# Performance work log

Measured on AMD Instinct MI355X. Metric: run time of the kernel, lower is better.

Reference implementation:

```python
import jax, jax.numpy as jnp
import numpy as np
import math

D_MODEL, N_HEADS, D_FF = 64, 8, 256
EPS = 1e-5


def _layernorm(x, w, b):
    mu = jnp.mean(x, axis=-1, keepdims=True)
    var = jnp.mean(jnp.square(x - mu), axis=-1, keepdims=True)
    return (x - mu) * jax.lax.rsqrt(var + EPS) * w + b


def setup_inputs() -> dict:
    key = jax.random.key(0)
    ks = jax.random.split(key, 16)
    B, S, D, F = 4, 2048, D_MODEL, D_FF
    s = 1.0 / math.sqrt(D)
    inp = {
        "x": jax.random.normal(ks[0], (B, S, D), jnp.float32),
        "mask": jax.random.randint(ks[1], (B, 1, S, S), 0, 2, jnp.int32),
        "Wq": jax.random.normal(ks[2], (D, D), jnp.float32) * s,
        "bq": jax.random.normal(ks[3], (D,), jnp.float32) * 0.02,
        "Wk": jax.random.normal(ks[4], (D, D), jnp.float32) * s,
        "bk": jax.random.normal(ks[5], (D,), jnp.float32) * 0.02,
        "Wv": jax.random.normal(ks[6], (D, D), jnp.float32) * s,
        "bv": jax.random.normal(ks[7], (D,), jnp.float32) * 0.02,
        "Wo": jax.random.normal(ks[8], (D, D), jnp.float32) * s,
        "bo": jax.random.normal(ks[9], (D,), jnp.float32) * 0.02,
        "W1": jax.random.normal(ks[10], (D, F), jnp.float32) * s,
        "b1": jax.random.normal(ks[11], (F,), jnp.float32) * 0.02,
        "W2": jax.random.normal(ks[12], (F, D), jnp.float32) * (1.0 / math.sqrt(F)),
        "b2": jax.random.normal(ks[13], (D,), jnp.float32) * 0.02,
        "ln1_w": jnp.ones((D,), jnp.float32),
        "ln1_b": jnp.zeros((D,), jnp.float32),
        "ln2_w": jnp.ones((D,), jnp.float32),
        "ln2_b": jnp.zeros((D,), jnp.float32),
    }
    return inp


def reference(x, mask, Wq, bq, Wk, bk, Wv, bv, Wo, bo, W1, b1, W2, b2,
              ln1_w, ln1_b, ln2_w, ln2_b):
    B, S, D = x.shape
    H = N_HEADS
    dk = D // H

    x1 = _layernorm(x, ln1_w, ln1_b)

    # [B,S,D] -> [B,H,S,dk]
    def heads(t):
        return t.reshape(B, S, H, dk).transpose(0, 2, 1, 3)

    Q = heads(x1 @ Wq + bq)
    K = heads(x1 @ Wk + bk)
    V = heads(x1 @ Wv + bv)

    scores = jnp.einsum("bhqd,bhkd->bhqk", Q, K) / math.sqrt(dk)
    scores = jnp.where(mask == 1, jnp.float32(-1e9), scores)
    attn = jax.nn.softmax(scores, axis=-1)
    ctx = jnp.einsum("bhqk,bhkd->bhqd", attn, V)
    # Faithful to source: view [B,H,S,dk] -> [B,S,D] WITHOUT transposing heads back.
    ctx = ctx.reshape(B, S, D)
    attn_out = ctx @ Wo + bo + x1  # residual added inside attention

    x2 = x1 + attn_out  # residual added again in the block (faithful double-add)
    x3 = _layernorm(x2, ln2_w, ln2_b)
    ff = jax.nn.gelu(x3 @ W1 + b1, approximate=False) @ W2 + b2
    return x2 + ff
```

## Files before the change

kernel.cpp:

```cpp
#include <hip/hip_runtime.h>
#include <hip/hip_bf16.h>

#define SEQ 2048

typedef short s4v __attribute__((ext_vector_type(4)));
typedef float f32x4 __attribute__((ext_vector_type(4)));

using bf16 = __hip_bfloat16;
using ull = unsigned long long;

#if __has_builtin(__builtin_amdgcn_exp2f)
#define EXP2(x) __builtin_amdgcn_exp2f(x)
#else
#define EXP2(x) exp2f(x)
#endif

__device__ __forceinline__ float wred_sum(float v){
#pragma unroll
  for (int i = 1; i < 64; i <<= 1) v += __shfl_xor(v, i, 64);
  return v;
}

__device__ __forceinline__ float wred_max(float v){
#pragma unroll
  for (int i = 1; i < 64; i <<= 1) v = fmaxf(v, __shfl_xor(v, i, 64));
  return v;
}

__device__ __forceinline__ short bfs(float f){
  bf16 h = __float2bfloat16(f);
  short s;
  __builtin_memcpy(&s, &h, 2);
  return s;
}

__device__ __forceinline__ unsigned bfs2(float a, float b){
  float2 t; t.x = a; t.y = b;
  __hip_bfloat162 h = __float22bfloat162_rn(t);
  unsigned u;
  __builtin_memcpy(&u, &h, 4);
  return u;
}

__device__ __forceinline__ int detect_f32(const void* xraw){
  const unsigned short* p = (const unsigned short*)xraw;
  const int lane = threadIdx.x & 63;
  float mx = 0.f;
#pragma unroll
  for (int i = 0; i < 2; ++i){
    unsigned u = ((unsigned)p[lane * 2 + i]) << 16;
    float f = fabsf(__uint_as_float(u));
    if (!(f < 1e30f)) f = 1e30f;
    mx = fmaxf(mx, f);
  }
  mx = wred_max(mx);
  return mx > 1e3f ? 1 : 0;
}

template<int F32>
__device__ __forceinline__ float ldf(const void* p, int i){
  if constexpr (F32) return ((const float*)p)[i];
  else return __bfloat162float(((const bf16*)p)[i]);
}

#define QSCALE 0.5101129340352065f

template<int F32>
__device__ __forceinline__ void ln_qkv_body(
    const void* x,
    const void* Wq, const void* bq,
    const void* Wk, const void* bk,
    const void* Wv, const void* bv,
    const void* ln1w, const void* ln1b,
    float* x1f, bf16* Qp, bf16* Kp, bf16* Vti, float (*xs)[64])
{
  const int w = threadIdx.x >> 6, lane = threadIdx.x & 63;
  const int row = (blockIdx.x - 2048) * 4 + w;
  float xv = ldf<F32>(x, row * 64 + lane);
  float mu = wred_sum(xv) * 0.015625f;
  float dv = xv - mu;
  float var = wred_sum(dv * dv) * 0.015625f;
  float x1 = dv * rsqrtf(var + 1e-5f) * ldf<F32>(ln1w, lane) + ldf<F32>(ln1b, lane);
  x1f[(size_t)row * 64 + lane] = x1;
  xs[w][lane] = x1;
  __syncthreads();
  float q = ldf<F32>(bq, lane);
  float k = ldf<F32>(bk, lane);
  float v = ldf<F32>(bv, lane);
#pragma unroll 16
  for (int d = 0; d < 64; ++d){
    float xd = xs[w][d];
    q += xd * ldf<F32>(Wq, d * 64 + lane);
    k += xd * ldf<F32>(Wk, d * 64 + lane);
    v += xd * ldf<F32>(Wv, d * 64 + lane);
  }
  const int bq_ = row >> 11, sq = row & 2047;
  const int hh = lane >> 3, dd = lane & 7;
  const int bh = bq_ * 8 + hh;
  const size_t pidx = ((size_t)bh * SEQ + sq) * 8 + dd;
  Qp[pidx] = __float2bfloat16(q * QSCALE);
  Kp[pidx] = __float2bfloat16(k);
  const int tt = sq >> 4, j = sq & 15;
  Vti[(((size_t)(bh * 128 + tt)) * 9 + dd) * 16 + j] = __float2bfloat16(v);
}

template<int F32>
__device__ __forceinline__ void wt_body(
    const void* Wo, const void* W1, const void* W2,
    bf16* WoT, bf16* W1T, bf16* W2T)
{
  const int idx = (blockIdx.x - 4096) * 256 + threadIdx.x;
  if (idx < 4096){
    const int c = idx >> 6, d = idx & 63;
    WoT[idx] = __float2bfloat16(ldf<F32>(Wo, d * 64 + c));
  } else if (idx < 20480){
    const int e = idx - 4096;
    const int f = e >> 6, d = e & 63;
    W1T[e] = __float2bfloat16(ldf<F32>(W1, d * 256 + f));
  } else {
    const int e = idx - 20480;
    const int c = e >> 8, f = e & 255;
    W2T[e] = __float2bfloat16(ldf<F32>(W2, f * 64 + c));
  }
}

__global__ __launch_bounds__(256) void k_prep(
    const int* __restrict__ mask, ull* __restrict__ pm,
    const void* x, const void* Wq, const void* bq, const void* Wk, const void* bk,
    const void* Wv, const void* bv, const void* ln1w, const void* ln1b,
    float* x1f, bf16* Qp, bf16* Kp, bf16* Vti,
    const void* Wo, const void* W1, const void* W2,
    bf16* WoT, bf16* W1T, bf16* W2T)
{
  __shared__ float xs[4][64];
  const int w = threadIdx.x >> 6, lane = threadIdx.x & 63;
  if (blockIdx.x < 2048){
    const int row = blockIdx.x * 4 + w;
    const int b = row >> 11, q = row & 2047;
    const int* rp = mask + (size_t)row * SEQ;
    ull* op = pm + ((size_t)(b * 128 + (q >> 4))) * 512 + (q & 15) * 2;
#pragma unroll
    for (int it = 0; it < 8; ++it){
      const int c0 = it * 256 + lane;
      ull m0 = __ballot(rp[c0] == 1);
      ull m1 = __ballot(rp[c0 + 64] == 1);
      ull m2 = __ballot(rp[c0 + 128] == 1);
      ull m3 = __ballot(rp[c0 + 192] == 1);
      if (lane == 0){
#pragma unroll
        for (int j = 0; j < 4; ++j){
          const int wi = it * 4 + j;
          const ull mv = (j == 0) ? m0 : (j == 1) ? m1 : (j == 2) ? m2 : m3;
          op[(wi >> 1) * 32 + (wi & 1)] = mv;
        }
      }
    }
    return;
  }
  if (blockIdx.x >= 4240){
    const int idx = (blockIdx.x - 4240) * 256 + threadIdx.x;
    const int bh = idx >> 11;
    const int rem = idx & 2047;
    const int tt = rem >> 4, j = rem & 15;
    Vti[(((size_t)(bh * 128 + tt)) * 9 + 8) * 16 + j] = __float2bfloat16(1.0f);
    return;
  }
  if (blockIdx.x >= 4096){
    if (detect_f32(x)) wt_body<1>(Wo, W1, W2, WoT, W1T, W2T);
    else               wt_body<0>(Wo, W1, W2, WoT, W1T, W2T);
    return;
  }
  if (detect_f32(x))
    ln_qkv_body<1>(x, Wq, bq, Wk, bk, Wv, bv, ln1w, ln1b, x1f, Qp, Kp, Vti, xs);
  else
    ln_qkv_body<0>(x, Wq, bq, Wk, bk, Wv, bv, ln1w, ln1b, x1f, Qp, Kp, Vti, xs);
}

#define LOADT(PB, T) do {                                                          \
    const int tt_ = (T);                                                           \
    _Pragma("unroll")                                                              \
    for (int i_ = 0; i_ < 8; ++i_){                                                \
      kf[PB][i_] = *reinterpret_cast<const s4v*>(kb8 + (size_t)(tt_ * 128 + i_ * 16) * 8); \
      vf[PB][i_] = *reinterpret_cast<const s4v*>(vb8 + (size_t)(tt_ * 8 + i_) * 144);      \
    }                                                                              \
    mwvA[PB] = pbA[tt_ * 16];                                                      \
    mwvB[PB] = pbB[tt_ * 16];                                                      \
  } while (0)

#define QTILE(PB, C, MM, QF, ACCA, ACCB) do {                                      \
    f32x4 st_[4];                                                                  \
    _Pragma("unroll")                                                              \
    for (int i_ = 0; i_ < 4; ++i_)                                                 \
      st_[i_] = __builtin_amdgcn_mfma_f32_16x16x16bf16_1k(kf[PB][(C) * 4 + i_], QF, zf, 0, 0, 0); \
    _Pragma("unroll")                                                              \
    for (int i_ = 0; i_ < 4; ++i_){                                                \
      const unsigned b4_ = (unsigned)((MM) >> (16 * i_ + sh4)) & 0xFu;             \
      float p0_ = (b4_ & 1u) ? 0.f : EXP2(st_[i_][0]);                             \
      float p1_ = (b4_ & 2u) ? 0.f : EXP2(st_[i_][1]);                             \
      float p2_ = (b4_ & 4u) ? 0.f : EXP2(st_[i_][2]);                             \
      float p3_ = (b4_ & 8u) ? 0.f : EXP2(st_[i_][3]);                             \
      union { unsigned u[2]; s4v s; } pu_;                                         \
      pu_.u[0] = bfs2(p0_, p1_);                                                   \
      pu_.u[1] = bfs2(p2_, p3_);                                                   \
      if (i_ & 1) ACCB = __builtin_amdgcn_mfma_f32_16x16x16bf16_1k(vf[PB][(C) * 4 + i_], pu_.s, ACCB, 0, 0, 0); \
      else        ACCA = __builtin_amdgcn_mfma_f32_16x16x16bf16_1k(vf[PB][(C) * 4 + i_], pu_.s, ACCA, 0, 0, 0); \
    }                                                                              \
  } while (0)

#define COMPT(PB) do {                                                             \
    const ull mxA_ = (((ull)mwvA[PB].y) << 32) | mwvA[PB].x;                       \
    const ull myA_ = (((ull)mwvA[PB].w) << 32) | mwvA[PB].z;                       \
    const ull mxB_ = (((ull)mwvB[PB].y) << 32) | mwvB[PB].x;                       \
    const ull myB_ = (((ull)mwvB[PB].w) << 32) | mwvB[PB].z;                       \
    QTILE(PB, 0, mxA_, qfA, accA0, accB0);                                         \
    QTILE(PB, 0, mxB_, qfB, accA1, accB1);                                         \
    QTILE(PB, 1, myA_, qfA, accA0, accB0);                                         \
    QTILE(PB, 1, myB_, qfB, accA1, accB1);                                         \
  } while (0)

__global__ __launch_bounds__(256, 4) void k_attn(
    const bf16* __restrict__ Qp, const bf16* __restrict__ Kp,
    const bf16* __restrict__ Vti, const uint4* __restrict__ pmi,
    bf16* __restrict__ ctxb)
{
  const int blk = blockIdx.x;
  const int h  = blk & 7;
  const int qt = (blk >> 3) & 63;
  const int b  = blk >> 9;
  const int kq = threadIdx.x >> 6;
  const int bh = b * 8 + h;
  const int q0 = qt * 32;
  const int lane = threadIdx.x & 63;
  const int g = lane >> 4, qi = lane & 15;
  const int sh4 = 4 * g;
  const int tbase = kq * 4;

  __shared__ float mlds[3][2][16][17];

  s4v qfA = {0, 0, 0, 0}, qfB = {0, 0, 0, 0};
  if (g < 2){
    qfA = *reinterpret_cast<const s4v*>(Qp + ((size_t)(bh * SEQ + q0 + qi)) * 8 + sh4);
    qfB = *reinterpret_cast<const s4v*>(Qp + ((size_t)(bh * SEQ + q0 + 16 + qi)) * 8 + sh4);
  }

  const bf16*  kb8 = Kp + ((size_t)bh * SEQ + qi) * 8 + sh4;
  const bf16*  vb8 = Vti + (size_t)bh * 128 * 144 + qi * 16 + sh4;
  const uint4* pbA = pmi + (size_t)(b * 128 + 2 * qt) * 256 + qi;
  const uint4* pbB = pbA + 256;

  f32x4 accA0 = {0.f, 0.f, 0.f, 0.f}, accB0 = {0.f, 0.f, 0.f, 0.f};
  f32x4 accA1 = {0.f, 0.f, 0.f, 0.f}, accB1 = {0.f, 0.f, 0.f, 0.f};
  const f32x4 zf = {0.f, 0.f, 0.f, 0.f};

  s4v kf[2][8], vf[2][8];
  uint4 mwvA[2], mwvB[2];

  LOADT(0, tbase);
  for (int it2 = 0; it2 < 2; ++it2){
    LOADT(1, tbase + ((2 * it2 + 1) & 3));
    COMPT(0);
    LOADT(0, tbase + ((2 * it2 + 2) & 3));
    COMPT(1);
  }

  f32x4 acc0, acc1;
#pragma unroll
  for (int r = 0; r < 4; ++r){
    acc0[r] = accA0[r] + accB0[r];
    acc1[r] = accA1[r] + accB1[r];
  }

  if (kq > 0){
#pragma unroll
    for (int r = 0; r < 4; ++r){
      mlds[kq - 1][0][4 * g + r][qi] = acc0[r];
      mlds[kq - 1][1][4 * g + r][qi] = acc1[r];
    }
  }
  __syncthreads();
  if (kq == 0){
#pragma unroll
    for (int j = 0; j < 3; ++j)
#pragma unroll
      for (int r = 0; r < 4; ++r){
        acc0[r] += mlds[j][0][4 * g + r][qi];
        acc1[r] += mlds[j][1][4 * g + r][qi];
      }
    const float s0 = __shfl(acc0[0], 32 + qi, 64);
    const float s1 = __shfl(acc1[0], 32 + qi, 64);
    if (g < 2){
      const float i0 = 1.f / s0, i1 = 1.f / s1;
      s4v oA, oB;
#pragma unroll
      for (int r = 0; r < 4; ++r){ oA[r] = bfs(acc0[r] * i0); oB[r] = bfs(acc1[r] * i1); }
      *reinterpret_cast<s4v*>(ctxb + ((size_t)(bh * SEQ + q0 + qi)) * 8 + sh4) = oA;
      *reinterpret_cast<s4v*>(ctxb + ((size_t)(bh * SEQ + q0 + 16 + qi)) * 8 + sh4) = oB;
    }
  }
}

template<int F32>
__device__ __forceinline__ void ffn_mfma_body(
    const bf16* __restrict__ ctxb, const float* __restrict__ x1f,
    const bf16* __restrict__ WoT, const bf16* __restrict__ W1T, const bf16* __restrict__ W2T,
    const void* bo, const void* b1, const void* b2,
    const void* ln2w, const void* ln2b, void* out)
{
  const int lane = threadIdx.x & 63;
  const int row0 = blockIdx.x * 16;
  const int xr = lane & 15;
  const int ko = (lane >> 4) * 4;
  const f32x4 zf = {0.f, 0.f, 0.f, 0.f};

  s4v cb[4];
#pragma unroll
  for (int kk = 0; kk < 4; ++kk)
    cb[kk] = *reinterpret_cast<const s4v*>(ctxb + (size_t)(row0 + xr) * 64 + kk * 16 + ko);

  float x2v[4][4];
#pragma unroll
  for (int t = 0; t < 4; ++t){
    f32x4 acc = zf;
#pragma unroll
    for (int kk = 0; kk < 4; ++kk){
      s4v a = *reinterpret_cast<const s4v*>(WoT + (size_t)(t * 16 + xr) * 64 + kk * 16 + ko);
      acc = __builtin_amdgcn_mfma_f32_16x16x16bf16_1k(a, cb[kk], acc, 0, 0, 0);
    }
    float4 x1q = *reinterpret_cast<const float4*>(x1f + (size_t)(row0 + xr) * 64 + t * 16 + ko);
#pragma unroll
    for (int r = 0; r < 4; ++r)
      x2v[t][r] = 2.f * (&x1q.x)[r] + acc[r] + ldf<F32>(bo, t * 16 + ko + r);
  }

  float s = 0.f;
#pragma unroll
  for (int t = 0; t < 4; ++t)
#pragma unroll
    for (int r = 0; r < 4; ++r) s += x2v[t][r];
  s += __shfl_xor(s, 16, 64);
  s += __shfl_xor(s, 32, 64);
  const float mu = s * 0.015625f;
  float vs = 0.f;
#pragma unroll
  for (int t = 0; t < 4; ++t)
#pragma unroll
    for (int r = 0; r < 4; ++r){ float d = x2v[t][r] - mu; vs += d * d; }
  vs += __shfl_xor(vs, 16, 64);
  vs += __shfl_xor(vs, 32, 64);
  const float rs = rsqrtf(vs * 0.015625f + 1e-5f);

  s4v xb[4];
#pragma unroll
  for (int t = 0; t < 4; ++t)
#pragma unroll
    for (int r = 0; r < 4; ++r)
      xb[t][r] = bfs((x2v[t][r] - mu) * rs * ldf<F32>(ln2w, t * 16 + ko + r)
                     + ldf<F32>(ln2b, t * 16 + ko + r));

  s4v gb[16];
#pragma unroll
  for (int u = 0; u < 16; ++u){
    f32x4 acc = zf;
#pragma unroll
    for (int t = 0; t < 4; ++t){
      s4v a = *reinterpret_cast<const s4v*>(W1T + (size_t)(u * 16 + xr) * 64 + t * 16 + ko);
      acc = __builtin_amdgcn_mfma_f32_16x16x16bf16_1k(a, xb[t], acc, 0, 0, 0);
    }
#pragma unroll
    for (int r = 0; r < 4; ++r){
      float h1 = acc[r] + ldf<F32>(b1, u * 16 + ko + r);
      gb[u][r] = bfs(0.5f * h1 * (1.f + erff(h1 * 0.70710678f)));
    }
  }

#pragma unroll
  for (int t = 0; t < 4; ++t){
    f32x4 acc = zf;
#pragma unroll
    for (int u = 0; u < 16; ++u){
      s4v a = *reinterpret_cast<const s4v*>(W2T + (size_t)(t * 16 + xr) * 256 + u * 16 + ko);
      acc = __builtin_amdgcn_mfma_f32_16x16x16bf16_1k(a, gb[u], acc, 0, 0, 0);
    }
    const size_t oidx = (size_t)(row0 + xr) * 64 + t * 16 + ko;
    if constexpr (F32){
      float4 o;
#pragma unroll
      for (int r = 0; r < 4; ++r)
        (&o.x)[r] = x2v[t][r] + acc[r] + ldf<F32>(b2, t * 16 + ko + r);
      *reinterpret_cast<float4*>((float*)out + oidx) = o;
    } else {
      s4v o;
#pragma unroll
      for (int r = 0; r < 4; ++r)
        o[r] = bfs(x2v[t][r] + acc[r] + ldf<F32>(b2, t * 16 + ko + r));
      *reinterpret_cast<s4v*>((bf16*)out + oidx) = o;
    }
  }
}

__global__ __launch_bounds__(64) void k_ffn(
    const void* xprobe,
    const bf16* __restrict__ ctxb, const float* __restrict__ x1f,
    const bf16* __restrict__ WoT, const bf16* __restrict__ W1T, const bf16* __restrict__ W2T,
    const void* bo, const void* b1, const void* b2,
    const void* ln2w, const void* ln2b, void* out)
{
  if (detect_f32(xprobe))
    ffn_mfma_body<1>(ctxb, x1f, WoT, W1T, W2T, bo, b1, b2, ln2w, ln2b, out);
  else
    ffn_mfma_body<0>(ctxb, x1f, WoT, W1T, W2T, bo, b1, b2, ln2w, ln2b, out);
}

extern "C" void kernel_launch(void* const* d_in, const int* in_sizes, int n_in,
                              void* d_out, int out_size, void* d_ws, size_t ws_size,
                              hipStream_t stream)
{
  (void)in_sizes; (void)n_in; (void)out_size; (void)ws_size;
  const void* x    = d_in[0];
  const int*  mask = (const int*)d_in[1];
  const void* Wq = d_in[2];
  const void* bq = d_in[3];
  const void* Wk = d_in[4];
  const void* bk = d_in[5];
  const void* Wv = d_in[6];
  const void* bv = d_in[7];
  const void* Wo = d_in[8];
  const void* bo = d_in[9];
  const void* W1 = d_in[10];
  const void* b1 = d_in[11];
  const void* W2 = d_in[12];
  const void* b2 = d_in[13];
  const void* ln1w = d_in[14];
  const void* ln1b = d_in[15];
  const void* ln2w = d_in[16];
  const void* ln2b = d_in[17];

  char* ws = (char*)d_ws;
  float* x1f = (float*)(ws + 0);
  bf16*  Qp  = (bf16*)(ws + (2u << 20));
  bf16*  Kp  = (bf16*)(ws + (3u << 20));
  bf16*  Vti = (bf16*)(ws + (5u << 20));
  bf16*  ctxb= (bf16*)(ws + (25u << 18));
  bf16*  WoT = (bf16*)(ws + (29u << 18));
  bf16*  W1T = (bf16*)(ws + (29u << 18) + 8192);
  bf16*  W2T = (bf16*)(ws + (29u << 18) + 40960);
  ull*   pm  = (ull*)(ws + (33u << 18));

  k_prep<<<4496, 256, 0, stream>>>(mask, pm, x, Wq, bq, Wk, bk, Wv, bv, ln1w, ln1b,
                                   x1f, Qp, Kp, Vti, Wo, W1, W2, WoT, W1T, W2T);
  k_attn<<<2048, 256, 0, stream>>>(Qp, Kp, Vti, (const uint4*)pm, ctxb);
  k_ffn<<<512, 64, 0, stream>>>(x, ctxb, x1f, WoT, W1T, W2T, bo, b1, b2, ln2w, ln2b, d_out);
}
```

Before: 90.74 us.

## Split FFN hidden dimension across four waves with LDS reduction

The FFN kernel now launches 256 threads per block instead of 64. Each wave computes a quarter of the 256-wide hidden layer (GELU plus its partial W2 product), and the partial outputs are summed through shared memory by wave 0. The attention kernel also reads the mask bits as 32-bit words instead of building 64-bit values, and fully unrolls the two-iteration tile loop. This spreads the FFN work over more waves to raise parallelism, at the cost of redundant Wo/LayerNorm work in every wave plus an LDS reduction and a barrier.

```diff
diff --git a/kernel.cpp b/kernel.cpp
--- a/kernel.cpp
+++ b/kernel.cpp
@@ -187,14 +187,15 @@
     mwvB[PB] = pbB[tt_ * 16];                                                      \
   } while (0)
 
-#define QTILE(PB, C, MM, QF, ACCA, ACCB) do {                                      \
+#define QTILE(PB, C, WLO, WHI, QF, ACCA, ACCB) do {                                \
     f32x4 st_[4];                                                                  \
     _Pragma("unroll")                                                              \
     for (int i_ = 0; i_ < 4; ++i_)                                                 \
       st_[i_] = __builtin_amdgcn_mfma_f32_16x16x16bf16_1k(kf[PB][(C) * 4 + i_], QF, zf, 0, 0, 0); \
     _Pragma("unroll")                                                              \
     for (int i_ = 0; i_ < 4; ++i_){                                                \
-      const unsigned b4_ = (unsigned)((MM) >> (16 * i_ + sh4)) & 0xFu;             \
+      const unsigned w32_ = (i_ < 2) ? (WLO) : (WHI);                              \
+      const unsigned b4_ = (w32_ >> (16 * (i_ & 1) + sh4)) & 0xFu;                 \
       float p0_ = (b4_ & 1u) ? 0.f : EXP2(st_[i_][0]);                             \
       float p1_ = (b4_ & 2u) ? 0.f : EXP2(st_[i_][1]);                             \
       float p2_ = (b4_ & 4u) ? 0.f : EXP2(st_[i_][2]);                             \
@@ -208,14 +209,10 @@
   } while (0)
 
 #define COMPT(PB) do {                                                             \
-    const ull mxA_ = (((ull)mwvA[PB].y) << 32) | mwvA[PB].x;                       \
-    const ull myA_ = (((ull)mwvA[PB].w) << 32) | mwvA[PB].z;                       \
-    const ull mxB_ = (((ull)mwvB[PB].y) << 32) | mwvB[PB].x;                       \
-    const ull myB_ = (((ull)mwvB[PB].w) << 32) | mwvB[PB].z;                       \
-    QTILE(PB, 0, mxA_, qfA, accA0, accB0);                                         \
-    QTILE(PB, 0, mxB_, qfB, accA1, accB1);                                         \
-    QTILE(PB, 1, myA_, qfA, accA0, accB0);                                         \
-    QTILE(PB, 1, myB_, qfB, accA1, accB1);                                         \
+    QTILE(PB, 0, mwvA[PB].x, mwvA[PB].y, qfA, accA0, accB0);                       \
+    QTILE(PB, 0, mwvB[PB].x, mwvB[PB].y, qfB, accA1, accB1);                       \
+    QTILE(PB, 1, mwvA[PB].z, mwvA[PB].w, qfA, accA0, accB0);                       \
+    QTILE(PB, 1, mwvB[PB].z, mwvB[PB].w, qfB, accA1, accB1);                       \
   } while (0)
 
 __global__ __launch_bounds__(256, 4) void k_attn(
@@ -256,6 +253,7 @@
   uint4 mwvA[2], mwvB[2];
 
   LOADT(0, tbase);
+#pragma unroll
   for (int it2 = 0; it2 < 2; ++it2){
     LOADT(1, tbase + ((2 * it2 + 1) & 3));
     COMPT(0);
@@ -304,9 +302,10 @@
     const bf16* __restrict__ ctxb, const float* __restrict__ x1f,
     const bf16* __restrict__ WoT, const bf16* __restrict__ W1T, const bf16* __restrict__ W2T,
     const void* bo, const void* b1, const void* b2,
-    const void* ln2w, const void* ln2b, void* out)
+    const void* ln2w, const void* ln2b, void* out, float (*mlds)[16][64])
 {
   const int lane = threadIdx.x & 63;
+  const int uq = threadIdx.x >> 6;
   const int row0 = blockIdx.x * 16;
   const int xr = lane & 15;
   const int ko = (lane >> 4) * 4;
@@ -357,9 +356,10 @@
       xb[t][r] = bfs((x2v[t][r] - mu) * rs * ldf<F32>(ln2w, t * 16 + ko + r)
                      + ldf<F32>(ln2b, t * 16 + ko + r));
 
-  s4v gb[16];
-#pragma unroll
-  for (int u = 0; u < 16; ++u){
+  s4v gb[4];
+#pragma unroll
+  for (int uu = 0; uu < 4; ++uu){
+    const int u = uq * 4 + uu;
     f32x4 acc = zf;
 #pragma unroll
     for (int t = 0; t < 4; ++t){
@@ -369,46 +369,69 @@
 #pragma unroll
     for (int r = 0; r < 4; ++r){
       float h1 = acc[r] + ldf<F32>(b1, u * 16 + ko + r);
-      gb[u][r] = bfs(0.5f * h1 * (1.f + erff(h1 * 0.70710678f)));
-    }
-  }
-
+      gb[uu][r] = bfs(0.5f * h1 * (1.f + erff(h1 * 0.70710678f)));
+    }
+  }
+
+  f32x4 oacc[4];
 #pragma unroll
   for (int t = 0; t < 4; ++t){
     f32x4 acc = zf;
 #pragma unroll
-    for (int u = 0; u < 16; ++u){
+    for (int uu = 0; uu < 4; ++uu){
+      const int u = uq * 4 + uu;
       s4v a = *reinterpret_cast<const s4v*>(W2T + (size_t)(t * 16 + xr) * 256 + u * 16 + ko);
-      acc = __builtin_amdgcn_mfma_f32_16x16x16bf16_1k(a, gb[u], acc, 0, 0, 0);
-    }
-    const size_t oidx = (size_t)(row0 + xr) * 64 + t * 16 + ko;
-    if constexpr (F32){
-      float4 o;
+      acc = __builtin_amdgcn_mfma_f32_16x16x16bf16_1k(a, gb[uu], acc, 0, 0, 0);
+    }
+    oacc[t] = acc;
+  }
+
+  if (uq > 0){
+#pragma unroll
+    for (int t = 0; t < 4; ++t)
 #pragma unroll
       for (int r = 0; r < 4; ++r)
-        (&o.x)[r] = x2v[t][r] + acc[r] + ldf<F32>(b2, t * 16 + ko + r);
-      *reinterpret_cast<float4*>((float*)out + oidx) = o;
-    } else {
-      s4v o;
-#pragma unroll
-      for (int r = 0; r < 4; ++r)
-        o[r] = bfs(x2v[t][r] + acc[r] + ldf<F32>(b2, t * 16 + ko + r));
-      *reinterpret_cast<s4v*>((bf16*)out + oidx) = o;
-    }
-  }
-}
-
-__global__ __launch_bounds__(64) void k_ffn(
+        mlds[uq - 1][xr][t * 16 + ko + r] = oacc[t][r];
+  }
+  __syncthreads();
+  if (uq == 0){
+#pragma unroll
+    for (int t = 0; t < 4; ++t){
+#pragma unroll
+      for (int j = 0; j < 3; ++j)
+#pragma unroll
+        for (int r = 0; r < 4; ++r)
+          oacc[t][r] += mlds[j][xr][t * 16 + ko + r];
+      const size_t oidx = (size_t)(row0 + xr) * 64 + t * 16 + ko;
+      if constexpr (F32){
+        float4 o;
+#pragma unroll
+        for (int r = 0; r < 4; ++r)
+          (&o.x)[r] = x2v[t][r] + oacc[t][r] + ldf<F32>(b2, t * 16 + ko + r);
+        *reinterpret_cast<float4*>((float*)out + oidx) = o;
+      } else {
+        s4v o;
+#pragma unroll
+        for (int r = 0; r < 4; ++r)
+          o[r] = bfs(x2v[t][r] + oacc[t][r] + ldf<F32>(b2, t * 16 + ko + r));
+        *reinterpret_cast<s4v*>((bf16*)out + oidx) = o;
+      }
+    }
+  }
+}
+
+__global__ __launch_bounds__(256) void k_ffn(
     const void* xprobe,
     const bf16* __restrict__ ctxb, const float* __restrict__ x1f,
     const bf16* __restrict__ WoT, const bf16* __restrict__ W1T, const bf16* __restrict__ W2T,
     const void* bo, const void* b1, const void* b2,
     const void* ln2w, const void* ln2b, void* out)
 {
+  __shared__ float mlds[3][16][64];
   if (detect_f32(xprobe))
-    ffn_mfma_body<1>(ctxb, x1f, WoT, W1T, W2T, bo, b1, b2, ln2w, ln2b, out);
+    ffn_mfma_body<1>(ctxb, x1f, WoT, W1T, W2T, bo, b1, b2, ln2w, ln2b, out, mlds);
   else
-    ffn_mfma_body<0>(ctxb, x1f, WoT, W1T, W2T, bo, b1, b2, ln2w, ln2b, out);
+    ffn_mfma_body<0>(ctxb, x1f, WoT, W1T, W2T, bo, b1, b2, ln2w, ln2b, out, mlds);
 }
 
 extern "C" void kernel_launch(void* const* d_in, const int* in_sizes, int n_in,
@@ -449,5 +472,5 @@
   k_prep<<<4496, 256, 0, stream>>>(mask, pm, x, Wq, bq, Wk, bk, Wv, bv, ln1w, ln1b,
                                    x1f, Qp, Kp, Vti, Wo, W1, W2, WoT, W1T, W2T);
   k_attn<<<2048, 256, 0, stream>>>(Qp, Kp, Vti, (const uint4*)pm, ctxb);
-  k_ffn<<<512, 64, 0, stream>>>(x, ctxb, x1f, WoT, W1T, W2T, bo, b1, b2, ln2w, ln2b, d_out);
-}
+  k_ffn<<<512, 256, 0, stream>>>(x, ctxb, x1f, WoT, W1T, W2T, bo, b1, b2, ln2w, ln2b, d_out);
+}
```

Result: faster. 81.28 us (median of 3 runs) (-10.4%).
